# Optimization experiments

Hardware: AMD Instinct MI355X
Metric: run time of the kernel (lower is better)

## Reference

```python
import jax, jax.numpy as jnp
import numpy as np

V, D, H, L, T_MAX = 95, 384, 6, 6, 256
HD = D // H  # 64
FF = 4 * D


def _layernorm(x, scale, bias, eps=1e-5):
    m = jnp.mean(x, axis=-1, keepdims=True)
    v = jnp.var(x, axis=-1, keepdims=True)
    return (x - m) * jax.lax.rsqrt(v + eps) * scale + bias


def setup_inputs() -> dict:
    key = jax.random.key(0)
    ks = iter(jax.random.split(key, 32))
    std = 0.02
    p = {
        "idx": jax.random.randint(next(ks), (128, 256), 0, V, dtype=jnp.int64)
               if jax.config.jax_enable_x64 else
               jax.random.randint(next(ks), (128, 256), 0, V, dtype=jnp.int32),
        "tok_emb": jax.random.normal(next(ks), (V, D), jnp.float32) * std,
        "pos_emb": jax.random.normal(next(ks), (T_MAX, D), jnp.float32) * std,
        # per-layer stacked params [L, ...]
        "ln1_s": jnp.ones((L, D), jnp.float32),
        "ln1_b": jnp.zeros((L, D), jnp.float32),
        "wq": jax.random.normal(next(ks), (L, D, D), jnp.float32) * std,
        "wk": jax.random.normal(next(ks), (L, D, D), jnp.float32) * std,
        "wv": jax.random.normal(next(ks), (L, D, D), jnp.float32) * std,
        "wo": jax.random.normal(next(ks), (L, D, D), jnp.float32) * std,
        "bo": jnp.zeros((L, D), jnp.float32),
        "ln2_s": jnp.ones((L, D), jnp.float32),
        "ln2_b": jnp.zeros((L, D), jnp.float32),
        "w1": jax.random.normal(next(ks), (L, D, FF), jnp.float32) * std,
        "b1": jnp.zeros((L, FF), jnp.float32),
        "w2": jax.random.normal(next(ks), (L, FF, D), jnp.float32) * std,
        "b2": jnp.zeros((L, D), jnp.float32),
        "lnf_s": jnp.ones((D,), jnp.float32),
        "lnf_b": jnp.zeros((D,), jnp.float32),
        "head_w": jax.random.normal(next(ks), (D, V), jnp.float32) * std,
        "head_b": jnp.zeros((V,), jnp.float32),
    }
    return p


def reference(idx, tok_emb, pos_emb, ln1_s, ln1_b, wq, wk, wv, wo, bo,
              ln2_s, ln2_b, w1, b1, w2, b2, lnf_s, lnf_b, head_w, head_b):
    B, T = idx.shape
    x = tok_emb[idx] + pos_emb[:T]  # [B,T,D]
    mask = jnp.tril(jnp.ones((T, T), bool))  # causal
    scale = HD ** -0.5

    def block(x, p):
        s1, b1n, Wq, Wk, Wv, Wo, Bo, s2, b2n, W1, B1, W2, B2 = p
        h = _layernorm(x, s1, b1n)
        q = (h @ Wq).reshape(B, T, H, HD)
        k = (h @ Wk).reshape(B, T, H, HD)
        v = (h @ Wv).reshape(B, T, H, HD)
        scores = jnp.einsum('bqhd,bkhd->bhqk', q, k) * scale
        scores = jnp.where(mask, scores, -jnp.inf)
        wei = jax.nn.softmax(scores, axis=-1)
        attn = jnp.einsum('bhqk,bkhd->bqhd', wei, v).reshape(B, T, D)
        x = x + attn @ Wo + Bo
        h2 = _layernorm(x, s2, b2n)
        x = x + jax.nn.relu(h2 @ W1 + B1) @ W2 + B2
        return x, None

    x, _ = jax.lax.scan(block, x, (ln1_s, ln1_b, wq, wk, wv, wo, bo,
                                   ln2_s, ln2_b, w1, b1, w2, b2))
    logits = _layernorm(x, lnf_s, lnf_b) @ head_w + head_b  # [B,T,V]
    return logits
```

## Files before the change

kernel.cpp:

```cpp
#include <hip/hip_runtime.h>
#include <hip/hip_bf16.h>
#include <cstdint>

#define DEV __device__ __forceinline__

typedef __hip_bfloat16 bf16;
typedef unsigned short u16;
typedef unsigned int u32;
typedef __attribute__((ext_vector_type(8))) short s8v;
typedef __attribute__((ext_vector_type(4))) float f4;

static constexpr int Bn = 128;
static constexpr int Tn = 256;
static constexpr int Dn = 384;
static constexpr int Hn = 6;
static constexpr int HDn = 64;
static constexpr int FFn = 1536;
static constexpr int Vn = 95;
static constexpr int Mn = Bn * 256;

DEV u16 f2b(float f) {
  bf16 h = __float2bfloat16(f);
  return *reinterpret_cast<u16*>(&h);
}
DEV u32 pk2(float a, float b) { return (u32)f2b(a) | ((u32)f2b(b) << 16); }

DEV void gl_lds16(const void* g, void* l) {
  auto gp = (const __attribute__((address_space(1))) u32*)(uintptr_t)g;
  auto lp = (__attribute__((address_space(3))) u32*)(u32)(uintptr_t)l;
  __builtin_amdgcn_global_load_lds(gp, lp, 16, 0, 0);
}

DEV void waitvm(int n) {
  if (n == 0)      asm volatile("s_waitcnt vmcnt(0)" ::: "memory");
  else if (n == 4) asm volatile("s_waitcnt vmcnt(4)" ::: "memory");
  else if (n == 8) asm volatile("s_waitcnt vmcnt(8)" ::: "memory");
}

template <int MODE, bool RELU, int NKT, int NT>
__global__ __launch_bounds__(256, 2) void gemm_h(
    const u16* __restrict__ A, const u16* __restrict__ Bw,
    const float* __restrict__ bias, const float* __restrict__ resid,
    void* __restrict__ outp)
{
  constexpr int K = NKT * 64;
  constexpr int N = NT * 16;
  constexpr int nTiles = NT / 8;
  __shared__ __align__(16) u16 As[3][128 * 64];
  const int tid = threadIdx.x;
  const int lane = tid & 63, wave = tid >> 6;
  const int quad = lane >> 4, l16 = lane & 15;
  const int wy = wave >> 1, wx = wave & 1;
  const int blk = blockIdx.x;
  const int xcd = blk & 7, tt = blk >> 3;
  const int nT = tt % nTiles, mT = xcd + 8 * (tt / nTiles);
  const int mBase = mT * 128, nBase = nT * 128;

  f4 acc[4][4] = {};

  int rS[4], cS[4];
#pragma unroll
  for (int i = 0; i < 4; i++) {
    int s = i * 256 + tid;
    rS[i] = s >> 3;
    cS[i] = ((s & 7) ^ (rS[i] & 7)) * 8;
  }

  const u16* Ab = A + (size_t)mBase * K;
  const u16* Bp = Bw + (size_t)((nBase >> 4) + wx * 4) * 512 + lane * 8;

#define STAGEA(buf, kt)                                                       \
  do {                                                                        \
    _Pragma("unroll")                                                         \
    for (int i = 0; i < 4; i++)                                               \
      gl_lds16(Ab + (size_t)rS[i] * K + (kt) + cS[i],                         \
               &As[buf][(i * 256 + wave * 64) * 8]);                          \
  } while (0)

  s8v bqa[2][4];
  STAGEA(0, 0);
  __builtin_amdgcn_sched_barrier(0);
#pragma unroll
  for (int j = 0; j < 4; j++)
    bqa[0][j] = *(const s8v*)(Bp + (size_t)0 * (NT * 512) + j * 512);
  __builtin_amdgcn_sched_barrier(0);
  STAGEA(1, 64);
  __builtin_amdgcn_sched_barrier(0);

  const int nk = NKT;
#pragma unroll
  for (int ik = 0; ik < nk; ik++) {
    const int cur = ik % 3;
    const int par = ik & 1;
    waitvm((ik + 1 < nk) ? 4 : 0);
    asm volatile("s_barrier" ::: "memory");
    s8v bqb[4];
#pragma unroll
    for (int j = 0; j < 4; j++)
      bqb[j] = *(const s8v*)(Bp + (size_t)(ik * 2 + 1) * (NT * 512) + j * 512);
    __builtin_amdgcn_sched_barrier(0);
    if (ik + 1 < nk) {
#pragma unroll
      for (int j = 0; j < 4; j++)
        bqa[par ^ 1][j] = *(const s8v*)(Bp + (size_t)(ik * 2 + 2) * (NT * 512) + j * 512);
    }
    __builtin_amdgcn_sched_barrier(0);
    if (ik + 2 < nk) STAGEA((ik + 2) % 3, (ik + 2) * 64);
    __builtin_amdgcn_sched_barrier(0);
    {
      s8v af[4];
#pragma unroll
      for (int i = 0; i < 4; i++) {
        int row = wy * 64 + i * 16 + l16;
        int ch = quad ^ (row & 7);
        af[i] = *(const s8v*)&As[cur][row * 64 + ch * 8];
      }
#pragma unroll
      for (int i = 0; i < 4; i++)
#pragma unroll
        for (int j = 0; j < 4; j++)
          acc[i][j] = __builtin_amdgcn_mfma_f32_16x16x32_bf16(af[i], bqa[par][j], acc[i][j], 0, 0, 0);
    }
    waitvm(4 * ((ik + 1 < nk) + (ik + 2 < nk)));
    {
      s8v af[4];
#pragma unroll
      for (int i = 0; i < 4; i++) {
        int row = wy * 64 + i * 16 + l16;
        int ch = (4 + quad) ^ (row & 7);
        af[i] = *(const s8v*)&As[cur][row * 64 + ch * 8];
      }
#pragma unroll
      for (int i = 0; i < 4; i++)
#pragma unroll
        for (int j = 0; j < 4; j++)
          acc[i][j] = __builtin_amdgcn_mfma_f32_16x16x32_bf16(af[i], bqb[j], acc[i][j], 0, 0, 0);
    }
  }
#undef STAGEA

  if (MODE == 0) {
    u16* out = (u16*)outp;
#pragma unroll
    for (int j = 0; j < 4; j++) {
      int n = nBase + wx * 64 + j * 16 + l16;
      float bv = bias ? bias[n] : 0.f;
#pragma unroll
      for (int i = 0; i < 4; i++) {
        int m0 = mBase + wy * 64 + i * 16 + quad * 4;
#pragma unroll
        for (int r = 0; r < 4; r++) {
          float v = acc[i][j][r] + bv;
          if (RELU) v = fmaxf(v, 0.f);
          out[(size_t)(m0 + r) * N + n] = f2b(v);
        }
      }
    }
  } else if (MODE == 1) {
    float* out = (float*)outp;
#pragma unroll
    for (int j = 0; j < 4; j++) {
      int n = nBase + wx * 64 + j * 16 + l16;
      float bv = bias[n];
#pragma unroll
      for (int i = 0; i < 4; i++) {
        int m0 = mBase + wy * 64 + i * 16 + quad * 4;
#pragma unroll
        for (int r = 0; r < 4; r++) {
          int m = m0 + r;
          out[(size_t)m * N + n] = resid[(size_t)m * N + n] + acc[i][j][r] + bv;
        }
      }
    }
  } else if (MODE == 3) {
    float* out = (float*)outp;
#pragma unroll
    for (int j = 0; j < 4; j++) {
      int n = nBase + wx * 64 + j * 16 + l16;
      if (n < Vn) {
        float bv = bias[n];
#pragma unroll
        for (int i = 0; i < 4; i++) {
          int m0 = mBase + wy * 64 + i * 16 + quad * 4;
#pragma unroll
          for (int r = 0; r < 4; r++)
            out[(size_t)(m0 + r) * Vn + n] = acc[i][j][r] + bv;
        }
      }
    }
  } else if (MODE == 4) {
    u16* qb = (u16*)outp;
    u16* kb = qb + (size_t)Mn * 384;
    u16* vb = kb + (size_t)Mn * 384;
#pragma unroll
    for (int j = 0; j < 4; j++) {
      int n = nBase + wx * 64 + j * 16 + l16;
      if (n < 768) {
        u16* dst = (n < 384) ? qb : kb;
        int col = (n < 384) ? n : (n - 384);
#pragma unroll
        for (int i = 0; i < 4; i++) {
          int m0 = mBase + wy * 64 + i * 16 + quad * 4;
#pragma unroll
          for (int r = 0; r < 4; r++)
            dst[(size_t)(m0 + r) * 384 + col] = f2b(acc[i][j][r]);
        }
      } else {
        int n7 = n - 768;
        int hh = n7 >> 6, d = n7 & 63;
#pragma unroll
        for (int i = 0; i < 4; i++) {
          int m0 = mBase + wy * 64 + i * 16 + quad * 4;
          int b = m0 >> 8, t0 = m0 & 255;
          uint2 w;
          w.x = pk2(acc[i][j][0], acc[i][j][1]);
          w.y = pk2(acc[i][j][2], acc[i][j][3]);
          *(uint2*)&vb[((b * Hn + hh) * HDn + d) * Tn + t0] = w;
        }
      }
    }
  }
}

__global__ __launch_bounds__(256) void attn_kernel(
    const u16* __restrict__ q, const u16* __restrict__ k,
    const u16* __restrict__ vT, u16* __restrict__ ao)
{
  __shared__ __align__(16) u16 Ps[4][2][16 * 40];
  const int tid = threadIdx.x, lane = tid & 63, wave = tid >> 6;
  const int quad = lane >> 4, l16 = lane & 15;
  const int c4 = blockIdx.x / 768;
  const int bh = blockIdx.x - c4 * 768;
  const int b = bh / Hn, h = bh % Hn;
  const u16* qg = q + (b * Tn) * Dn + h * HDn;
  const u16* kg = k + (b * Tn) * Dn + h * HDn;
  const u16* vg = vT + bh * (HDn * Tn);
  u16* aog = ao + (b * Tn) * Dn + h * HDn;
  const float c1 = 0.125f * 1.44269504f;

  const int qt = (wave & 2) ? ((wave & 1) ? 15 - c4 : 8 + c4)
                            : ((wave & 1) ? 7 - c4 : c4);
  const int qglob = qt * 16 + l16;

  const s8v qf0 = *(const s8v*)&qg[qglob * Dn + quad * 8];
  const s8v qf1 = *(const s8v*)&qg[qglob * Dn + 32 + quad * 8];

  float lsum = 0.f;
  f4 O[4] = {};

  const int nch = qt / 2 + 1;
  for (int c2 = 0; c2 < nch; c2++) {
    const int kk0 = c2 * 32;
    f4 S0 = {0.f, 0.f, 0.f, 0.f}, S1 = S0;
    {
      s8v kf = *(const s8v*)&kg[(kk0 + l16) * Dn + quad * 8];
      S0 = __builtin_amdgcn_mfma_f32_16x16x32_bf16(kf, qf0, S0, 0, 0, 0);
      kf = *(const s8v*)&kg[(kk0 + l16) * Dn + 32 + quad * 8];
      S0 = __builtin_amdgcn_mfma_f32_16x16x32_bf16(kf, qf1, S0, 0, 0, 0);
    }
    if (kk0 + 16 <= qt * 16) {
      s8v kf = *(const s8v*)&kg[(kk0 + 16 + l16) * Dn + quad * 8];
      S1 = __builtin_amdgcn_mfma_f32_16x16x32_bf16(kf, qf0, S1, 0, 0, 0);
      kf = *(const s8v*)&kg[(kk0 + 16 + l16) * Dn + 32 + quad * 8];
      S1 = __builtin_amdgcn_mfma_f32_16x16x32_bf16(kf, qf1, S1, 0, 0, 0);
    }
    const int kkq = kk0 + quad * 4;
    f4 E0, E1;
#pragma unroll
    for (int r = 0; r < 4; r++) {
      E0[r] = (kkq + r <= qglob) ? exp2f(S0[r] * c1) : 0.f;
      E1[r] = (kkq + 16 + r <= qglob) ? exp2f(S1[r] * c1) : 0.f;
      lsum += E0[r] + E1[r];
    }
    u16* prow = &Ps[wave][c2 & 1][l16 * 40];
    uint2 w0, w1;
    w0.x = pk2(E0[0], E0[1]); w0.y = pk2(E0[2], E0[3]);
    w1.x = pk2(E1[0], E1[1]); w1.y = pk2(E1[2], E1[3]);
    *(uint2*)&prow[quad * 4] = w0;
    *(uint2*)&prow[16 + quad * 4] = w1;
    const s8v pf = *(const s8v*)&prow[quad * 8];
#pragma unroll
    for (int dm = 0; dm < 4; dm++) {
      s8v vf = *(const s8v*)&vg[(dm * 16 + l16) * Tn + kk0 + quad * 8];
      O[dm] = __builtin_amdgcn_mfma_f32_16x16x32_bf16(vf, pf, O[dm], 0, 0, 0);
    }
  }

  lsum += __shfl_xor(lsum, 16);
  lsum += __shfl_xor(lsum, 32);
  const float inv = 1.0f / lsum;
#pragma unroll
  for (int dm = 0; dm < 4; dm++) {
    uint2 w;
    w.x = pk2(O[dm][0] * inv, O[dm][1] * inv);
    w.y = pk2(O[dm][2] * inv, O[dm][3] * inv);
    *(uint2*)&aog[qglob * Dn + dm * 16 + quad * 4] = w;
  }
}

__global__ __launch_bounds__(256) void ln_kernel(
    const float* __restrict__ x, const float* __restrict__ sc,
    const float* __restrict__ bi, u16* __restrict__ out)
{
  int tok = blockIdx.x * 4 + (threadIdx.x >> 6);
  int lane = threadIdx.x & 63;
  const float* xr = x + (size_t)tok * Dn;
  float v[6];
  float s = 0.f, sq = 0.f;
#pragma unroll
  for (int i = 0; i < 6; i++) {
    v[i] = xr[lane + 64 * i];
    s += v[i];
    sq += v[i] * v[i];
  }
#pragma unroll
  for (int o = 1; o < 64; o <<= 1) {
    s += __shfl_xor(s, o);
    sq += __shfl_xor(sq, o);
  }
  float mean = s * (1.f / 384.f);
  float var = sq * (1.f / 384.f) - mean * mean;
  float inv = rsqrtf(var + 1e-5f);
  u16* orow = out + (size_t)tok * Dn;
#pragma unroll
  for (int i = 0; i < 6; i++) {
    int c = lane + 64 * i;
    orow[c] = f2b((v[i] - mean) * inv * sc[c] + bi[c]);
  }
}

__global__ __launch_bounds__(256) void embed_kernel(
    const int* __restrict__ idx, const float* __restrict__ tok,
    const float* __restrict__ pos, float* __restrict__ x)
{
  int i = blockIdx.x * 256 + threadIdx.x;
  int m = i / 96, c = (i - m * 96) * 4;
  int t = m & (Tn - 1);
  const float4 tv = *(const float4*)&tok[idx[m] * Dn + c];
  const float4 pv = *(const float4*)&pos[t * Dn + c];
  float4 r;
  r.x = tv.x + pv.x; r.y = tv.y + pv.y; r.z = tv.z + pv.z; r.w = tv.w + pv.w;
  *(float4*)&x[m * Dn + c] = r;
}

__global__ __launch_bounds__(256) void tcvt_frag(
    const float* __restrict__ src, u16* __restrict__ dst,
    int K, int C, int NTsub, int NTtot, int ntoff, int total)
{
  int t = blockIdx.x * 256 + threadIdx.x;
  if (t >= total) return;
  int j8 = t & 7;
  int lane = (t >> 3) & 63;
  int rest = t >> 9;
  int nt = rest % NTsub;
  int lkc = rest / NTsub;
  int KC = K >> 5;
  int kc = lkc % KC;
  int l = lkc / KC;
  int quad = lane >> 4, l16 = lane & 15;
  int k = kc * 32 + quad * 8 + j8;
  int n = nt * 16 + l16;
  float v = (n < C) ? src[((size_t)l * K + k) * C + n] : 0.f;
  dst[((size_t)(l * KC + kc) * NTtot + ntoff + nt) * 512 + lane * 8 + j8] = f2b(v);
}

extern "C" void kernel_launch(void* const* d_in, const int* in_sizes, int n_in,
                              void* d_out, int out_size, void* d_ws, size_t ws_size,
                              hipStream_t stream)
{
  (void)in_sizes; (void)n_in; (void)out_size;
  const int*   idx     = (const int*)d_in[0];
  const float* tok_emb = (const float*)d_in[1];
  const float* pos_emb = (const float*)d_in[2];
  const float* ln1_s   = (const float*)d_in[3];
  const float* ln1_b   = (const float*)d_in[4];
  const float* wq      = (const float*)d_in[5];
  const float* wk      = (const float*)d_in[6];
  const float* wv      = (const float*)d_in[7];
  const float* wo      = (const float*)d_in[8];
  const float* bo      = (const float*)d_in[9];
  const float* ln2_s   = (const float*)d_in[10];
  const float* ln2_b   = (const float*)d_in[11];
  const float* w1      = (const float*)d_in[12];
  const float* b1      = (const float*)d_in[13];
  const float* w2      = (const float*)d_in[14];
  const float* b2      = (const float*)d_in[15];
  const float* lnf_s   = (const float*)d_in[16];
  const float* lnf_b   = (const float*)d_in[17];
  const float* head_w  = (const float*)d_in[18];
  const float* head_b  = (const float*)d_in[19];
  float* out = (float*)d_out;

  char* ws = (char*)d_ws;
  float* x  = (float*)(ws + 0);
  u16*   h  = (u16*)(ws + 50331648);
  u16*   qb = (u16*)(ws + 75497472);
  u16*   kb = (u16*)(ws + 100663296);
  u16*   vb = (u16*)(ws + 125829120);
  u16*   ab = (u16*)(ws + 150994944);
  u16*   f1 = qb;
  u16* qkvT = (u16*)(ws + 176160768);
  u16* woT  = qkvT + 6 * 442368;
  u16* w1T  = woT + 6 * 147456;
  u16* w2T  = w1T + 6 * 589824;
  u16* hdT  = w2T + 6 * 589824;
  if (ws_size < (size_t)197492736) return;

  int tot = 6 * 384 * 384;
  tcvt_frag<<<(tot + 255) / 256, 256, 0, stream>>>(wq, qkvT, 384, 384, 24, 72, 0, tot);
  tcvt_frag<<<(tot + 255) / 256, 256, 0, stream>>>(wk, qkvT, 384, 384, 24, 72, 24, tot);
  tcvt_frag<<<(tot + 255) / 256, 256, 0, stream>>>(wv, qkvT, 384, 384, 24, 72, 48, tot);
  tcvt_frag<<<(tot + 255) / 256, 256, 0, stream>>>(wo, woT, 384, 384, 24, 24, 0, tot);
  tot = 6 * 384 * 1536;
  tcvt_frag<<<(tot + 255) / 256, 256, 0, stream>>>(w1, w1T, 384, 1536, 96, 96, 0, tot);
  tcvt_frag<<<(tot + 255) / 256, 256, 0, stream>>>(w2, w2T, 1536, 384, 24, 24, 0, tot);
  tot = 384 * 128;
  tcvt_frag<<<(tot + 255) / 256, 256, 0, stream>>>(head_w, hdT, 384, 95, 8, 8, 0, tot);

  embed_kernel<<<(Mn * 96) / 256, 256, 0, stream>>>(idx, tok_emb, pos_emb, x);

  for (int l = 0; l < 6; l++) {
    ln_kernel<<<Mn / 4, 256, 0, stream>>>(x, ln1_s + l * Dn, ln1_b + l * Dn, h);
    gemm_h<4, false, 6, 72><<<2304, 256, 0, stream>>>(h, qkvT + l * 442368, nullptr, nullptr, qb);
    attn_kernel<<<Bn * Hn * 4, 256, 0, stream>>>(qb, kb, vb, ab);
    gemm_h<1, false, 6, 24><<<768, 256, 0, stream>>>(ab, woT + l * 147456, bo + l * Dn, x, x);
    ln_kernel<<<Mn / 4, 256, 0, stream>>>(x, ln2_s + l * Dn, ln2_b + l * Dn, h);
    gemm_h<0, true, 6, 96><<<3072, 256, 0, stream>>>(h, w1T + l * 589824, b1 + l * FFn, nullptr, f1);
    gemm_h<1, false, 24, 24><<<768, 256, 0, stream>>>(f1, w2T + l * 589824, b2 + l * Dn, x, x);
  }
  ln_kernel<<<Mn / 4, 256, 0, stream>>>(x, lnf_s, lnf_b, h);
  gemm_h<3, false, 6, 8><<<256, 256, 0, stream>>>(h, hdT, head_b, nullptr, out);
}
```

Baseline: 1.602 ms.

## Fuse residual-add GEMMs with following LayerNorm in full-row tiles

Adds a gemm_ln kernel that computes a 128x384 full-row output tile per 512-thread block. It writes the residual-updated x and then computes the LayerNorm of those rows in the epilogue through a cross-wave shared-memory reduction, emitting bf16 h directly. This removes the separate ln_kernel launches and their re-read of x after the Wo and W2 projections, with the next layer's ln1 (or the final LN) folded into the W2 GEMM. The cost is only 256 blocks per GEMM, which lowers parallelism, and variance is computed as E[x^2]-mean^2 instead of two-pass.

```diff
diff --git a/kernel.cpp b/kernel.cpp
--- a/kernel.cpp
+++ b/kernel.cpp
@@ -32,9 +32,13 @@
 }
 
 DEV void waitvm(int n) {
-  if (n == 0)      asm volatile("s_waitcnt vmcnt(0)" ::: "memory");
-  else if (n == 4) asm volatile("s_waitcnt vmcnt(4)" ::: "memory");
-  else if (n == 8) asm volatile("s_waitcnt vmcnt(8)" ::: "memory");
+  if (n == 0)       asm volatile("s_waitcnt vmcnt(0)" ::: "memory");
+  else if (n == 2)  asm volatile("s_waitcnt vmcnt(2)" ::: "memory");
+  else if (n == 4)  asm volatile("s_waitcnt vmcnt(4)" ::: "memory");
+  else if (n == 6)  asm volatile("s_waitcnt vmcnt(6)" ::: "memory");
+  else if (n == 8)  asm volatile("s_waitcnt vmcnt(8)" ::: "memory");
+  else if (n == 12) asm volatile("s_waitcnt vmcnt(12)" ::: "memory");
+  else              asm volatile("s_waitcnt vmcnt(16)" ::: "memory");
 }
 
 template <int MODE, bool RELU, int NKT, int NT>
@@ -156,22 +160,6 @@
         }
       }
     }
-  } else if (MODE == 1) {
-    float* out = (float*)outp;
-#pragma unroll
-    for (int j = 0; j < 4; j++) {
-      int n = nBase + wx * 64 + j * 16 + l16;
-      float bv = bias[n];
-#pragma unroll
-      for (int i = 0; i < 4; i++) {
-        int m0 = mBase + wy * 64 + i * 16 + quad * 4;
-#pragma unroll
-        for (int r = 0; r < 4; r++) {
-          int m = m0 + r;
-          out[(size_t)m * N + n] = resid[(size_t)m * N + n] + acc[i][j][r] + bv;
-        }
-      }
-    }
   } else if (MODE == 3) {
     float* out = (float*)outp;
 #pragma unroll
@@ -220,6 +208,167 @@
       }
     }
   }
+}
+
+template <int NKT>
+__global__ __launch_bounds__(512, 2) void gemm_ln(
+    const u16* __restrict__ A, const u16* __restrict__ Bw,
+    const float* __restrict__ bias, const float* __restrict__ resid,
+    float* __restrict__ xout,
+    const float* __restrict__ sc, const float* __restrict__ bi,
+    u16* __restrict__ hout)
+{
+  constexpr int K = NKT * 64;
+  constexpr int NT = 24;
+  __shared__ __align__(16) u16 As[3][128 * 64];
+  __shared__ float2 red[4][128];
+  const int tid = threadIdx.x;
+  const int lane = tid & 63, wave = tid >> 6;
+  const int quad = lane >> 4, l16 = lane & 15;
+  const int wy = wave >> 2, wx = wave & 3;
+  const int blk = blockIdx.x;
+  const int mT = (blk & 7) + 8 * (blk >> 3);
+  const int mBase = mT * 128;
+
+  f4 acc[4][6] = {};
+
+  int rS[2], cS[2];
+#pragma unroll
+  for (int i = 0; i < 2; i++) {
+    int s = i * 512 + tid;
+    rS[i] = s >> 3;
+    cS[i] = ((s & 7) ^ (rS[i] & 7)) * 8;
+  }
+
+  const u16* Ab = A + (size_t)mBase * K;
+  const u16* Bp = Bw + (size_t)(wx * 6) * 512 + lane * 8;
+
+#define STAGEL(buf, kt)                                                       \
+  do {                                                                        \
+    _Pragma("unroll")                                                         \
+    for (int i = 0; i < 2; i++)                                               \
+      gl_lds16(Ab + (size_t)rS[i] * K + (kt) + cS[i],                         \
+               &As[buf][(i * 512 + wave * 64) * 8]);                          \
+  } while (0)
+
+  STAGEL(0, 0);
+  __builtin_amdgcn_sched_barrier(0);
+  STAGEL(1, 64);
+  __builtin_amdgcn_sched_barrier(0);
+
+  const int nk = NKT;
+#pragma unroll
+  for (int ik = 0; ik < nk; ik++) {
+    const int cur = ik % 3;
+    waitvm((ik + 1 < nk) ? 2 : 0);
+    asm volatile("s_barrier" ::: "memory");
+    s8v bq0[6], bq1[6];
+#pragma unroll
+    for (int j = 0; j < 6; j++)
+      bq0[j] = *(const s8v*)(Bp + (size_t)(ik * 2) * (NT * 512) + j * 512);
+    __builtin_amdgcn_sched_barrier(0);
+#pragma unroll
+    for (int j = 0; j < 6; j++)
+      bq1[j] = *(const s8v*)(Bp + (size_t)(ik * 2 + 1) * (NT * 512) + j * 512);
+    __builtin_amdgcn_sched_barrier(0);
+    if (ik + 2 < nk) STAGEL((ik + 2) % 3, (ik + 2) * 64);
+    __builtin_amdgcn_sched_barrier(0);
+    waitvm(6 + ((ik + 2 < nk) ? 2 : 0));
+    {
+      s8v af[4];
+#pragma unroll
+      for (int i = 0; i < 4; i++) {
+        int row = wy * 64 + i * 16 + l16;
+        int ch = quad ^ (row & 7);
+        af[i] = *(const s8v*)&As[cur][row * 64 + ch * 8];
+      }
+#pragma unroll
+      for (int i = 0; i < 4; i++)
+#pragma unroll
+        for (int j = 0; j < 6; j++)
+          acc[i][j] = __builtin_amdgcn_mfma_f32_16x16x32_bf16(af[i], bq0[j], acc[i][j], 0, 0, 0);
+    }
+    waitvm((ik + 2 < nk) ? 2 : 0);
+    {
+      s8v af[4];
+#pragma unroll
+      for (int i = 0; i < 4; i++) {
+        int row = wy * 64 + i * 16 + l16;
+        int ch = (4 + quad) ^ (row & 7);
+        af[i] = *(const s8v*)&As[cur][row * 64 + ch * 8];
+      }
+#pragma unroll
+      for (int i = 0; i < 4; i++)
+#pragma unroll
+        for (int j = 0; j < 6; j++)
+          acc[i][j] = __builtin_amdgcn_mfma_f32_16x16x32_bf16(af[i], bq1[j], acc[i][j], 0, 0, 0);
+    }
+  }
+#undef STAGEL
+
+  f4 psum[4] = {}, psq[4] = {};
+#pragma unroll
+  for (int j = 0; j < 6; j++) {
+    int n = wx * 96 + j * 16 + l16;
+    float bv = bias[n];
+#pragma unroll
+    for (int i = 0; i < 4; i++) {
+      int m0 = mBase + wy * 64 + i * 16 + quad * 4;
+#pragma unroll
+      for (int r = 0; r < 4; r++) {
+        int m = m0 + r;
+        float v = resid[(size_t)m * Dn + n] + acc[i][j][r] + bv;
+        xout[(size_t)m * Dn + n] = v;
+        acc[i][j][r] = v;
+        psum[i][r] += v;
+        psq[i][r] += v * v;
+      }
+    }
+  }
+#pragma unroll
+  for (int o = 1; o < 16; o <<= 1)
+#pragma unroll
+    for (int i = 0; i < 4; i++)
+#pragma unroll
+      for (int r = 0; r < 4; r++) {
+        psum[i][r] += __shfl_xor(psum[i][r], o);
+        psq[i][r] += __shfl_xor(psq[i][r], o);
+      }
+  if (l16 == 0) {
+#pragma unroll
+    for (int i = 0; i < 4; i++)
+#pragma unroll
+      for (int r = 0; r < 4; r++) {
+        int lr = wy * 64 + i * 16 + quad * 4 + r;
+        float2 p; p.x = psum[i][r]; p.y = psq[i][r];
+        red[wx][lr] = p;
+      }
+  }
+  __syncthreads();
+  float scv[6], biv[6];
+#pragma unroll
+  for (int j = 0; j < 6; j++) {
+    int n = wx * 96 + j * 16 + l16;
+    scv[j] = sc[n];
+    biv[j] = bi[n];
+  }
+#pragma unroll
+  for (int i = 0; i < 4; i++)
+#pragma unroll
+    for (int r = 0; r < 4; r++) {
+      int lr = wy * 64 + i * 16 + quad * 4 + r;
+      float ts = 0.f, tq = 0.f;
+#pragma unroll
+      for (int w = 0; w < 4; w++) { float2 p = red[w][lr]; ts += p.x; tq += p.y; }
+      float mean = ts * (1.f / 384.f);
+      float inv = rsqrtf(tq * (1.f / 384.f) - mean * mean + 1e-5f);
+      int m = mBase + lr;
+#pragma unroll
+      for (int j = 0; j < 6; j++) {
+        int n = wx * 96 + j * 16 + l16;
+        hout[(size_t)m * Dn + n] = f2b((acc[i][j][r] - mean) * inv * scv[j] + biv[j]);
+      }
+    }
 }
 
 __global__ __launch_bounds__(256) void attn_kernel(
@@ -418,16 +567,18 @@
   tcvt_frag<<<(tot + 255) / 256, 256, 0, stream>>>(head_w, hdT, 384, 95, 8, 8, 0, tot);
 
   embed_kernel<<<(Mn * 96) / 256, 256, 0, stream>>>(idx, tok_emb, pos_emb, x);
+  ln_kernel<<<Mn / 4, 256, 0, stream>>>(x, ln1_s, ln1_b, h);
 
   for (int l = 0; l < 6; l++) {
-    ln_kernel<<<Mn / 4, 256, 0, stream>>>(x, ln1_s + l * Dn, ln1_b + l * Dn, h);
     gemm_h<4, false, 6, 72><<<2304, 256, 0, stream>>>(h, qkvT + l * 442368, nullptr, nullptr, qb);
     attn_kernel<<<Bn * Hn * 4, 256, 0, stream>>>(qb, kb, vb, ab);
-    gemm_h<1, false, 6, 24><<<768, 256, 0, stream>>>(ab, woT + l * 147456, bo + l * Dn, x, x);
-    ln_kernel<<<Mn / 4, 256, 0, stream>>>(x, ln2_s + l * Dn, ln2_b + l * Dn, h);
+    gemm_ln<6><<<256, 512, 0, stream>>>(ab, woT + l * 147456, bo + l * Dn, x, x,
+                                        ln2_s + l * Dn, ln2_b + l * Dn, h);
     gemm_h<0, true, 6, 96><<<3072, 256, 0, stream>>>(h, w1T + l * 589824, b1 + l * FFn, nullptr, f1);
-    gemm_h<1, false, 24, 24><<<768, 256, 0, stream>>>(f1, w2T + l * 589824, b2 + l * Dn, x, x);
-  }
-  ln_kernel<<<Mn / 4, 256, 0, stream>>>(x, lnf_s, lnf_b, h);
+    const float* ns = (l < 5) ? (ln1_s + (l + 1) * Dn) : lnf_s;
+    const float* nb = (l < 5) ? (ln1_b + (l + 1) * Dn) : lnf_b;
+    gemm_ln<24><<<256, 512, 0, stream>>>(f1, w2T + l * 589824, b2 + l * Dn, x, x,
+                                         ns, nb, h);
+  }
   gemm_h<3, false, 6, 8><<<256, 256, 0, stream>>>(h, hdT, head_b, nullptr, out);
 }
```

After: 1.609 ms. About the same (+0.4%).
